# Kernel optimization log

Hardware: AMD Instinct MI355X
Metric: run time of the kernel (lower is better)

The kernel has to match this reference:

```python
import jax, jax.numpy as jnp
import numpy as np

B, N, M, D = 16, 4096, 4096, 3

def setup_inputs() -> dict:
    key = jax.random.key(0)
    k1, k2 = jax.random.split(key)
    x = jax.random.normal(k1, (B, N, D), dtype=jnp.float32)
    y = jax.random.normal(k2, (B, M, D), dtype=jnp.float32)
    return {"x": x, "y": y}

def reference(x, y):
    # pairwise L2 distance matrix C: [B, N, M]
    diff = x[:, :, None, :] - y[:, None, :, :]          # [B, N, M, D]
    C = jnp.sqrt(jnp.sum(diff * diff, axis=-1))          # [B, N, M]
    d1 = jnp.min(C, axis=-1).mean(axis=-1)               # x -> nearest y, mean over N: [B]
    d2 = jnp.min(C, axis=-2).mean(axis=-1)               # y -> nearest x, mean over M: [B]
    cost = (d1 + d2) / 2.0                               # reduction='none'
    return cost
```

## Files before the change

### kernel.cpp

```cpp
#include <hip/hip_runtime.h>
#include <cstdint>
#include <cstddef>

#define S      4096
#define BATCH  16
#define BLK    256
#define YSPAN  2048
#define CHUNK  512
#define NTILE  (CHUNK / 32)
#define NCHUNK (YSPAN / CHUNK)
#define ROWS_PER_BLOCK 128
#define XC_N   (S / ROWS_PER_BLOCK)
#define YC_N   (S / YSPAN)

typedef _Float16 half8   __attribute__((ext_vector_type(8)));
typedef float    floatx16 __attribute__((ext_vector_type(16)));

__device__ inline unsigned pack2(_Float16 lo, _Float16 hi) {
    unsigned short a = __builtin_bit_cast(unsigned short, lo);
    unsigned short b = __builtin_bit_cast(unsigned short, hi);
    return (unsigned)a | ((unsigned)b << 16);
}

__global__ __launch_bounds__(BLK) void chamfer_mfma_kernel(
    const float* __restrict__ x, const float* __restrict__ y,
    float* __restrict__ ws0, float* __restrict__ ws1,
    float* __restrict__ out)
{
    const int b    = blockIdx.y;
    const int xc   = blockIdx.x;
    const int yc   = blockIdx.z;
    const int tid  = threadIdx.x;
    const int lane = tid & 63;
    const int wave = tid >> 6;
    const int hi32 = lane >> 5;
    const int l31  = lane & 31;

    if (xc == 0 && yc == 0 && tid == 0) out[b] = 0.0f;

    __shared__ uint4    ldsb[2][NTILE][64];
    __shared__ unsigned colmin[YSPAN];

    for (int i = tid; i < YSPAN; i += BLK) colmin[i] = 0x7F7F7F7Fu;
    for (int i = tid; i < 2 * NTILE * 32; i += BLK) {
        int bu = i / (NTILE * 32); int r = i % (NTILE * 32);
        ldsb[bu][r >> 5][32 + (r & 31)].z = 0x00003C00u;
        ldsb[bu][r >> 5][32 + (r & 31)].w = 0u;
    }

    const int row = xc * ROWS_PER_BLOCK + wave * 32 + l31;
    const float* xp = x + ((size_t)b * S + row) * 3;
    const float x0 = xp[0], x1 = xp[1], x2 = xp[2];
    const float xn = 0.5f * (x0 * x0 + x1 * x1 + x2 * x2);
    const _Float16 xh0 = (_Float16)x0, xh1 = (_Float16)x1, xh2 = (_Float16)x2;
    const _Float16 xl0 = (_Float16)(x0 - (float)xh0);
    const _Float16 xl1 = (_Float16)(x1 - (float)xh1);
    const _Float16 xl2 = (_Float16)(x2 - (float)xh2);
    const _Float16 xnh = (_Float16)xn;
    const _Float16 xnl = (_Float16)(xn - (float)xnh);
    half8 afrag;
    if (hi32 == 0) {
        afrag[0] = -xh0; afrag[1] = -xh1; afrag[2] = -xh2;
        afrag[3] = -xh0; afrag[4] = -xh1; afrag[5] = -xh2;
        afrag[6] = -xl0; afrag[7] = -xl1;
    } else {
        afrag[0] = -xl2; afrag[1] = (_Float16)1.0f; afrag[2] = (_Float16)1.0f;
        afrag[3] = xnh;  afrag[4] = xnl;
        afrag[5] = (_Float16)0.0f; afrag[6] = (_Float16)0.0f; afrag[7] = (_Float16)0.0f;
    }

    floatx16 runrow;
#pragma unroll
    for (int r = 0; r < 16; ++r) runrow[r] = 3.0e38f;
    const floatx16 zeroacc = {};

    const int ybase = yc * YSPAN;
    const float* ysrc = y + ((size_t)b * S + ybase) * 3;

    auto stage = [&](int cc) {
        const int buf = cc & 1;
#pragma unroll
        for (int q = 0; q < 2; ++q) {
            const int pl = tid * 2 + q;
            const int p  = cc * CHUNK + pl;
            const float* yp = ysrc + (size_t)p * 3;
            const float y0 = yp[0], y1 = yp[1], y2 = yp[2];
            const float h  = 0.5f * (y0 * y0 + y1 * y1 + y2 * y2);
            const _Float16 a0 = (_Float16)y0, a1 = (_Float16)y1, a2 = (_Float16)y2;
            const _Float16 b0 = (_Float16)(y0 - (float)a0);
            const _Float16 b1 = (_Float16)(y1 - (float)a1);
            const _Float16 b2 = (_Float16)(y2 - (float)a2);
            const _Float16 hh = (_Float16)h;
            const _Float16 hl = (_Float16)(h - (float)hh);
            const int t = pl >> 5, col = pl & 31;
            ldsb[buf][t][col] = make_uint4(pack2(a0, a1), pack2(a2, b0),
                                           pack2(b1, b2), pack2(a0, a1));
            *(uint2*)&ldsb[buf][t][32 + col] =
                make_uint2(pack2(a2, hh), pack2(hl, (_Float16)1.0f));
        }
    };

    stage(0);
    __syncthreads();

    for (int c = 0; c < NCHUNK; ++c) {
        if (c + 1 < NCHUNK) stage(c + 1);
        const int buf = c & 1;
#pragma unroll 4
        for (int t = 0; t < NTILE; ++t) {
            const uint4 braw = ldsb[buf][t][lane];
            const half8 bfrag = __builtin_bit_cast(half8, braw);
            const floatx16 d =
                __builtin_amdgcn_mfma_f32_32x32x16_f16(afrag, bfrag, zeroacc, 0, 0, 0);
#pragma unroll
            for (int r = 0; r < 16; ++r) runrow[r] = fminf(runrow[r], d[r]);
            float m = fminf(fminf(d[0], d[1]), d[2]);
            m = fminf(fminf(m, d[3]), d[4]);
            m = fminf(fminf(m, d[5]), d[6]);
            m = fminf(fminf(m, d[7]), d[8]);
            m = fminf(fminf(m, d[9]), d[10]);
            m = fminf(fminf(m, d[11]), d[12]);
            m = fminf(fminf(m, d[13]), d[14]);
            m = fminf(m, d[15]);
            m = fminf(m, __shfl_xor(m, 32));
            m = fmaxf(m, 0.0f);
            if (lane < 32)
                atomicMin(&colmin[c * CHUNK + t * 32 + l31], __float_as_uint(m));
        }
        __syncthreads();
    }

#pragma unroll
    for (int r = 0; r < 16; ++r) {
        float v = runrow[r];
        v = fminf(v, __shfl_xor(v, 1));
        v = fminf(v, __shfl_xor(v, 2));
        v = fminf(v, __shfl_xor(v, 4));
        v = fminf(v, __shfl_xor(v, 8));
        v = fminf(v, __shfl_xor(v, 16));
        runrow[r] = v;
    }
    if (l31 == 0) {
        float* w0 = ws0 + ((size_t)yc * BATCH + b) * S
                        + xc * ROWS_PER_BLOCK + wave * 32;
#pragma unroll
        for (int r = 0; r < 16; ++r) {
            const int rr = (r & 3) + 8 * (r >> 2) + 4 * hi32;
            w0[rr] = fmaxf(runrow[r], 0.0f);
        }
    }

    float* w1 = ws1 + ((size_t)xc * BATCH + b) * S + ybase;
    for (int i = tid; i < YSPAN; i += BLK)
        w1[i] = __uint_as_float(colmin[i]);
}

#define RSEG   (S / BLK)
__global__ __launch_bounds__(BLK) void chamfer_reduce_kernel(
    const float* __restrict__ ws0, const float* __restrict__ ws1,
    float* __restrict__ out)
{
    const int b   = blockIdx.y;
    const int i   = blockIdx.x * BLK + threadIdx.x;
    const int tid = threadIdx.x;

    const float mx = fminf(ws0[(size_t)b * S + i],
                           ws0[((size_t)BATCH + b) * S + i]);
    float my = 3.0e38f;
#pragma unroll
    for (int xc = 0; xc < XC_N; ++xc)
        my = fminf(my, ws1[((size_t)xc * BATCH + b) * S + i]);

    float s = sqrtf(2.0f * mx) + sqrtf(2.0f * my);

    __shared__ float red[BLK];
    red[tid] = s;
    __syncthreads();
    for (int off = BLK / 2; off > 0; off >>= 1) {
        if (tid < off) red[tid] += red[tid + off];
        __syncthreads();
    }
    if (tid == 0) atomicAdd(&out[b], red[0] * (0.5f / (float)S));
}

#define P   8
#define FMC 1024
#define OUTER_PER_BLK (BLK * P)
__global__ __launch_bounds__(BLK) void chamfer_full_kernel(
    const float* __restrict__ x, const float* __restrict__ y,
    float* __restrict__ out)
{
    const int role = blockIdx.z;
    const int b    = blockIdx.y;
    const int oc   = blockIdx.x;
    const float* __restrict__ outer = (role == 0) ? x : y;
    const float* __restrict__ inner = (role == 0) ? y : x;
    const int tid = threadIdx.x;
    const int n0  = oc * OUTER_PER_BLK;

    __shared__ float4 lds[FMC];

    float nx0[P], nx1[P], nx2[P], xn[P], tmin[P];
#pragma unroll
    for (int p = 0; p < P; ++p) {
        const int n = n0 + p * BLK + tid;
        const float* xp = outer + ((size_t)b * S + n) * 3;
        const float a0 = xp[0], a1 = xp[1], a2 = xp[2];
        nx0[p] = -a0; nx1[p] = -a1; nx2[p] = -a2;
        xn[p]  = a0 * a0 + a1 * a1 + a2 * a2;
        tmin[p] = 3.0e38f;
    }

    for (int m0 = 0; m0 < S; m0 += FMC) {
        __syncthreads();
        for (int i = tid; i < FMC; i += BLK) {
            const float* yp = inner + ((size_t)b * S + m0 + i) * 3;
            const float a0 = yp[0], a1 = yp[1], a2 = yp[2];
            lds[i] = make_float4(a0, a1, a2,
                                 0.5f * (a0 * a0 + a1 * a1 + a2 * a2));
        }
        __syncthreads();
#pragma unroll 4
        for (int j = 0; j < FMC; ++j) {
            const float4 v = lds[j];
#pragma unroll
            for (int p = 0; p < P; ++p) {
                const float t = fmaf(nx0[p], v.x,
                                 fmaf(nx1[p], v.y,
                                  fmaf(nx2[p], v.z, v.w)));
                tmin[p] = fminf(tmin[p], t);
            }
        }
    }

    float s = 0.0f;
#pragma unroll
    for (int p = 0; p < P; ++p)
        s += sqrtf(fmaxf(fmaf(2.0f, tmin[p], xn[p]), 0.0f));

    __shared__ float red[BLK];
    red[tid] = s;
    __syncthreads();
    for (int off = BLK / 2; off > 0; off >>= 1) {
        if (tid < off) red[tid] += red[tid + off];
        __syncthreads();
    }
    if (tid == 0) atomicAdd(&out[b], red[0] * (0.5f / (float)S));
}

extern "C" void kernel_launch(void* const* d_in, const int* in_sizes, int n_in,
                              void* d_out, int out_size, void* d_ws, size_t ws_size,
                              hipStream_t stream) {
    const float* x = (const float*)d_in[0];
    const float* y = (const float*)d_in[1];
    float* out = (float*)d_out;

    const size_t n_ws0 = (size_t)YC_N * BATCH * S;
    const size_t n_ws1 = (size_t)XC_N * BATCH * S;
    const size_t need  = (n_ws0 + n_ws1) * sizeof(float);
    if (ws_size >= need) {
        float* ws0 = (float*)d_ws;
        float* ws1 = ws0 + n_ws0;
        chamfer_mfma_kernel<<<dim3(XC_N, BATCH, YC_N), BLK, 0, stream>>>(
            x, y, ws0, ws1, out);
        chamfer_reduce_kernel<<<dim3(RSEG, BATCH), BLK, 0, stream>>>(
            ws0, ws1, out);
    } else {
        hipMemsetAsync(d_out, 0, BATCH * sizeof(float), stream);
        chamfer_full_kernel<<<dim3(S / OUTER_PER_BLK, BATCH, 2), BLK, 0, stream>>>(
            x, y, out);
    }
}
```

Before: 40.72 us.

## Halve Y span per block, drop cross-half shuffle, fully unroll tile loop

Halves the Y span per block (and the chunk size), which doubles the grid along the Y dimension to give more blocks for occupancy, and adds a launch-bounds hint of 5 blocks per CU. Each thread now stages one y point instead of two. The column-min no longer shuffles across the two 32-lane halves; both halves do LDS atomicMin directly. The in-tile min is rebuilt as a shallower tree and the tile loop is fully unrolled. The reduce kernel now loops over YC_N partials. The trade-off is more LDS atomics, more partial rows written to the workspace, and more reduce work.

```diff
diff --git a/kernel.cpp b/kernel.cpp
--- a/kernel.cpp
+++ b/kernel.cpp
@@ -5,8 +5,8 @@
 #define S      4096
 #define BATCH  16
 #define BLK    256
-#define YSPAN  2048
-#define CHUNK  512
+#define YSPAN  1024
+#define CHUNK  256
 #define NTILE  (CHUNK / 32)
 #define NCHUNK (YSPAN / CHUNK)
 #define ROWS_PER_BLOCK 128
@@ -22,7 +22,7 @@
     return (unsigned)a | ((unsigned)b << 16);
 }
 
-__global__ __launch_bounds__(BLK) void chamfer_mfma_kernel(
+__global__ __launch_bounds__(BLK, 5) void chamfer_mfma_kernel(
     const float* __restrict__ x, const float* __restrict__ y,
     float* __restrict__ ws0, float* __restrict__ ws1,
     float* __restrict__ out)
@@ -79,25 +79,21 @@
 
     auto stage = [&](int cc) {
         const int buf = cc & 1;
-#pragma unroll
-        for (int q = 0; q < 2; ++q) {
-            const int pl = tid * 2 + q;
-            const int p  = cc * CHUNK + pl;
-            const float* yp = ysrc + (size_t)p * 3;
-            const float y0 = yp[0], y1 = yp[1], y2 = yp[2];
-            const float h  = 0.5f * (y0 * y0 + y1 * y1 + y2 * y2);
-            const _Float16 a0 = (_Float16)y0, a1 = (_Float16)y1, a2 = (_Float16)y2;
-            const _Float16 b0 = (_Float16)(y0 - (float)a0);
-            const _Float16 b1 = (_Float16)(y1 - (float)a1);
-            const _Float16 b2 = (_Float16)(y2 - (float)a2);
-            const _Float16 hh = (_Float16)h;
-            const _Float16 hl = (_Float16)(h - (float)hh);
-            const int t = pl >> 5, col = pl & 31;
-            ldsb[buf][t][col] = make_uint4(pack2(a0, a1), pack2(a2, b0),
-                                           pack2(b1, b2), pack2(a0, a1));
-            *(uint2*)&ldsb[buf][t][32 + col] =
-                make_uint2(pack2(a2, hh), pack2(hl, (_Float16)1.0f));
-        }
+        const int p   = cc * CHUNK + tid;
+        const float* yp = ysrc + (size_t)p * 3;
+        const float y0 = yp[0], y1 = yp[1], y2 = yp[2];
+        const float h  = 0.5f * (y0 * y0 + y1 * y1 + y2 * y2);
+        const _Float16 a0 = (_Float16)y0, a1 = (_Float16)y1, a2 = (_Float16)y2;
+        const _Float16 b0 = (_Float16)(y0 - (float)a0);
+        const _Float16 b1 = (_Float16)(y1 - (float)a1);
+        const _Float16 b2 = (_Float16)(y2 - (float)a2);
+        const _Float16 hh = (_Float16)h;
+        const _Float16 hl = (_Float16)(h - (float)hh);
+        const int t = tid >> 5, col = tid & 31;
+        ldsb[buf][t][col] = make_uint4(pack2(a0, a1), pack2(a2, b0),
+                                       pack2(b1, b2), pack2(a0, a1));
+        *(uint2*)&ldsb[buf][t][32 + col] =
+            make_uint2(pack2(a2, hh), pack2(hl, (_Float16)1.0f));
     };
 
     stage(0);
@@ -106,7 +102,7 @@
     for (int c = 0; c < NCHUNK; ++c) {
         if (c + 1 < NCHUNK) stage(c + 1);
         const int buf = c & 1;
-#pragma unroll 4
+#pragma unroll
         for (int t = 0; t < NTILE; ++t) {
             const uint4 braw = ldsb[buf][t][lane];
             const half8 bfrag = __builtin_bit_cast(half8, braw);
@@ -114,18 +110,16 @@
                 __builtin_amdgcn_mfma_f32_32x32x16_f16(afrag, bfrag, zeroacc, 0, 0, 0);
 #pragma unroll
             for (int r = 0; r < 16; ++r) runrow[r] = fminf(runrow[r], d[r]);
-            float m = fminf(fminf(d[0], d[1]), d[2]);
-            m = fminf(fminf(m, d[3]), d[4]);
-            m = fminf(fminf(m, d[5]), d[6]);
-            m = fminf(fminf(m, d[7]), d[8]);
-            m = fminf(fminf(m, d[9]), d[10]);
-            m = fminf(fminf(m, d[11]), d[12]);
-            m = fminf(fminf(m, d[13]), d[14]);
+            const float m1 = fminf(fminf(d[0],  d[1]),  d[2]);
+            const float m2 = fminf(fminf(d[3],  d[4]),  d[5]);
+            const float m3 = fminf(fminf(d[6],  d[7]),  d[8]);
+            const float m4 = fminf(fminf(d[9],  d[10]), d[11]);
+            const float m5 = fminf(fminf(d[12], d[13]), d[14]);
+            float m = fminf(fminf(m1, m2), m3);
+            m = fminf(fminf(m, m4), m5);
             m = fminf(m, d[15]);
-            m = fminf(m, __shfl_xor(m, 32));
             m = fmaxf(m, 0.0f);
-            if (lane < 32)
-                atomicMin(&colmin[c * CHUNK + t * 32 + l31], __float_as_uint(m));
+            atomicMin(&colmin[c * CHUNK + t * 32 + l31], __float_as_uint(m));
         }
         __syncthreads();
     }
@@ -164,8 +158,10 @@
     const int i   = blockIdx.x * BLK + threadIdx.x;
     const int tid = threadIdx.x;
 
-    const float mx = fminf(ws0[(size_t)b * S + i],
-                           ws0[((size_t)BATCH + b) * S + i]);
+    float mx = 3.0e38f;
+#pragma unroll
+    for (int yc = 0; yc < YC_N; ++yc)
+        mx = fminf(mx, ws0[((size_t)yc * BATCH + b) * S + i]);
     float my = 3.0e38f;
 #pragma unroll
     for (int xc = 0; xc < XC_N; ++xc)
```

Result: faster. 35.89 us (-11.9%).
